# Kernel tuning notes

Hardware: AMD Instinct MI355X
Metric: run time of the kernel (lower is better)

## Reference

```python
import jax, jax.numpy as jnp
import numpy as np

N = 100000      # nodes
E = 1600000     # nnz of precomputed A^K (avg degree 16)
D = 64          # in_feats
C = 64          # n_classes
LN_EPS = 1e-5


def setup_inputs() -> dict:
    key = jax.random.key(0)
    ks = jax.random.split(key, 8)
    feat = jax.random.normal(ks[0], (N, D), dtype=jnp.float32)
    feat_ori = jax.random.normal(ks[1], (N, D), dtype=jnp.float32)
    row = jax.random.randint(ks[2], (E,), 0, N)
    col = jax.random.randint(ks[3], (E,), 0, N)
    adj_vals = jax.random.uniform(ks[4], (E,), dtype=jnp.float32)
    # Linear params (xavier_uniform weight, zero bias)
    limit = float(np.sqrt(6.0 / (D + C)))
    W = jax.random.uniform(ks[5], (C, D), dtype=jnp.float32, minval=-limit, maxval=limit)
    b = jnp.zeros((C,), dtype=jnp.float32)
    # LayerNorm params
    gamma = jnp.ones((C,), dtype=jnp.float32)
    beta = jnp.zeros((C,), dtype=jnp.float32)
    return {"feat": feat, "feat_ori": feat_ori, "row": row, "col": col,
            "adj_vals": adj_vals, "W": W, "b": b, "gamma": gamma, "beta": beta}


def reference(feat, feat_ori, row, col, adj_vals, W, b, gamma, beta):
    # NOTE: in the source, h = (1-alpha)*feat + alpha*feat_ori is dead code
    # (immediately overwritten by the SpMM of raw feat), so it is omitted.
    # SpMM: h[i] = sum_{e: row[e]=i} adj_vals[e] * feat[col[e]]   -> [N, D]
    msgs = adj_vals[:, None] * feat[col]            # [E, D] gather + scale
    h = jax.ops.segment_sum(msgs, row, num_segments=N)  # [N, D] scatter-add
    # Dense Linear: [N, D] @ [D, C] + [C]
    h = jnp.einsum('nd,cd->nc', h, W) + b
    # LayerNorm over last dim
    mu = jnp.mean(h, axis=-1, keepdims=True)
    var = jnp.mean(jnp.square(h - mu), axis=-1, keepdims=True)
    h = (h - mu) * jax.lax.rsqrt(var + LN_EPS) * gamma + beta
    return h
```

## Files before the change

### kernel.cpp

```cpp
#include <hip/hip_runtime.h>


typedef unsigned int u32;
typedef unsigned short u16;
typedef unsigned long long u64;
#define RFL(x) __builtin_amdgcn_readfirstlane(x)

#define NBLKC 64
#define MAXBK 2048
#define CAP 2048

__device__ __forceinline__ float bf2f(u16 v) {
    return __uint_as_float((u32)v << 16);
}
__device__ __forceinline__ u16 f2bf(float f) {
    u32 b = __float_as_uint(f);
    return (u16)((b + 0x7FFFu + ((b >> 16) & 1u)) >> 16);
}

__global__ __launch_bounds__(256) void k_bhist(const int* __restrict__ row,
                                               u32* __restrict__ hist2d,
                                               int E, int NBK, int CH) {
    __shared__ u32 cnt[MAXBK];
    int tid = threadIdx.x;
    for (int i = tid; i < NBK; i += 256) cnt[i] = 0;
    __syncthreads();
    int e0 = blockIdx.x * CH;
    int e1 = e0 + CH; if (e1 > E) e1 = E;
    int ev = e1 & ~3;
    for (int i = e0 + tid * 4; i < ev; i += 1024) {
        int4 r = *reinterpret_cast<const int4*>(&row[i]);
        atomicAdd(&cnt[(u32)r.x >> 6], 1u);
        atomicAdd(&cnt[(u32)r.y >> 6], 1u);
        atomicAdd(&cnt[(u32)r.z >> 6], 1u);
        atomicAdd(&cnt[(u32)r.w >> 6], 1u);
    }
    { int i = ev + tid; if (i < e1) atomicAdd(&cnt[(u32)row[i] >> 6], 1u); }
    __syncthreads();
    u32* dst = hist2d + (size_t)blockIdx.x * NBK;
    for (int i = tid; i < NBK; i += 256) dst[i] = cnt[i];
}

__device__ __forceinline__ u32 blk_scan256(u32 v, u32* wsum, u32& total) {
    int lane = threadIdx.x & 63, wid = threadIdx.x >> 6;
    u32 incl = v;
#pragma unroll
    for (int o = 1; o < 64; o <<= 1) {
        u32 u = __shfl_up(incl, o);
        if (lane >= o) incl += u;
    }
    if (lane == 63) wsum[wid] = incl;
    __syncthreads();
    u32 woff = 0;
    for (int w = 0; w < wid; ++w) woff += wsum[w];
    total = wsum[0] + wsum[1] + wsum[2] + wsum[3];
    __syncthreads();
    return woff + incl - v;
}

__global__ __launch_bounds__(256) void k_bscan(u32* __restrict__ hist2d,
                                               u32* __restrict__ btot,
                                               int NBLK, int NBK) {
    __shared__ u32 wsum[4];
    int bkt = blockIdx.x;
    u32 carry = 0;
    for (int r = 0; r < NBLK; r += 256) {
        int blk = r + threadIdx.x;
        u32 v = (blk < NBLK) ? hist2d[(size_t)blk * NBK + bkt] : 0;
        u32 tot;
        u32 ex = blk_scan256(v, wsum, tot);
        if (blk < NBLK) hist2d[(size_t)blk * NBK + bkt] = ex + carry;
        carry += tot;
    }
    if (threadIdx.x == 0) btot[bkt] = carry;
}

__global__ __launch_bounds__(256) void k_scanb2(const u32* __restrict__ btot,
                                                u32* __restrict__ bbase,
                                                int NBK, int E) {
    __shared__ u32 wsum[4];
    u32 carry = 0;
    for (int r = 0; r < NBK; r += 256) {
        int i = r + threadIdx.x;
        u32 v = (i < NBK) ? btot[i] : 0;
        u32 tot;
        u32 ex = blk_scan256(v, wsum, tot);
        if (i < NBK) bbase[i] = ex + carry;
        carry += tot;
    }
    if (threadIdx.x == 0) bbase[NBK] = (u32)E;
}

__global__ __launch_bounds__(512) void k_scatgemm(
    const int* __restrict__ row, const int* __restrict__ col,
    const float* __restrict__ vals, const u32* __restrict__ hist2d,
    const u32* __restrict__ bbase, u64* __restrict__ epair1,
    const float* __restrict__ feat, const float* __restrict__ W,
    u16* __restrict__ G, int E, int N, int NBK, int NBLK, int CH)
{
    __shared__ __align__(16) u32 smem[8192];
    int tid = threadIdx.x;
    if ((int)blockIdx.x < NBLK) {
        u32* lbase = smem;
        u32* lcnt  = smem + NBK;
        int blk = blockIdx.x;
        const u32* hrow = hist2d + (size_t)blk * NBK;
        for (int i = tid; i < NBK; i += 512) {
            lbase[i] = bbase[i] + hrow[i];
            lcnt[i] = 0;
        }
        __syncthreads();
        int e0 = blk * CH;
        int e1 = e0 + CH; if (e1 > E) e1 = E;
        int ev = e1 & ~3;
        for (int i = e0 + tid * 4; i < ev; i += 2048) {
            int4 r = *reinterpret_cast<const int4*>(&row[i]);
            int4 c = *reinterpret_cast<const int4*>(&col[i]);
            float4 v = *reinterpret_cast<const float4*>(&vals[i]);
            u32 k0 = (u32)r.x >> 6, k1 = (u32)r.y >> 6;
            u32 k2 = (u32)r.z >> 6, k3 = (u32)r.w >> 6;
            u32 q0 = atomicAdd(&lcnt[k0], 1u);
            u32 q1 = atomicAdd(&lcnt[k1], 1u);
            u32 q2 = atomicAdd(&lcnt[k2], 1u);
            u32 q3 = atomicAdd(&lcnt[k3], 1u);
            epair1[lbase[k0] + q0] = (u64)((u32)c.x | (((u32)r.x & 63u) << 26))
                                   | ((u64)__float_as_uint(v.x) << 32);
            epair1[lbase[k1] + q1] = (u64)((u32)c.y | (((u32)r.y & 63u) << 26))
                                   | ((u64)__float_as_uint(v.y) << 32);
            epair1[lbase[k2] + q2] = (u64)((u32)c.z | (((u32)r.z & 63u) << 26))
                                   | ((u64)__float_as_uint(v.z) << 32);
            epair1[lbase[k3] + q3] = (u64)((u32)c.w | (((u32)r.w & 63u) << 26))
                                   | ((u64)__float_as_uint(v.w) << 32);
        }
        {
            int i = ev + tid;
            if (i < e1) {
                u32 r = (u32)row[i];
                u32 k = r >> 6;
                u32 q = atomicAdd(&lcnt[k], 1u);
                epair1[lbase[k] + q] = (u64)((u32)col[i] | ((r & 63u) << 26))
                                     | ((u64)__float_as_uint(vals[i]) << 32);
            }
        }
    } else {
        float* fs = (float*)smem;
        int lane = tid & 63, wid = tid >> 6;
        int n0 = ((int)blockIdx.x - NBLK) * 128;
        int valid = N - n0; if (valid > 128) valid = 128;
        int elems = valid * 64;
        for (int idx = tid * 4; idx < elems; idx += 2048)
            *reinterpret_cast<float4*>(&fs[idx]) =
                *reinterpret_cast<const float4*>(&feat[(size_t)n0 * 64 + idx]);
        float wr[64];
#pragma unroll
        for (int d4 = 0; d4 < 16; ++d4) {
            float4 w4 = *reinterpret_cast<const float4*>(&W[lane * 64 + d4 * 4]);
            wr[d4 * 4 + 0] = w4.x; wr[d4 * 4 + 1] = w4.y;
            wr[d4 * 4 + 2] = w4.z; wr[d4 * 4 + 3] = w4.w;
        }
        __syncthreads();
        for (int j = 0; j < 16; ++j) {
            int r = wid * 16 + j;
            if (r >= valid) break;
            float oa[4] = {0.f, 0.f, 0.f, 0.f};
#pragma unroll
            for (int d4 = 0; d4 < 16; ++d4) {
                float4 h4 = *reinterpret_cast<const float4*>(&fs[r * 64 + d4 * 4]);
                oa[d4 & 3] = fmaf(h4.x, wr[d4 * 4 + 0],
                            fmaf(h4.y, wr[d4 * 4 + 1],
                            fmaf(h4.z, wr[d4 * 4 + 2],
                            fmaf(h4.w, wr[d4 * 4 + 3], oa[d4 & 3]))));
            }
            G[(size_t)(n0 + r) * 64 + lane] = f2bf((oa[0] + oa[1]) + (oa[2] + oa[3]));
        }
    }
}

__global__ __launch_bounds__(256) void k_node2(
    const u16* __restrict__ G, const u64* __restrict__ epair1,
    const u32* __restrict__ bbase, const float* __restrict__ bias,
    const float* __restrict__ gamma, const float* __restrict__ beta,
    float* __restrict__ out, int N)
{
    __shared__ u64 sp[CAP];
    __shared__ u32 cnt[64], base[64], cnt2[64];
    int tid = threadIdx.x, lane = tid & 63, wid = tid >> 6;
    int bkt = blockIdx.x;
    if (tid < 64) { cnt[tid] = 0; cnt2[tid] = 0; }
    __syncthreads();
    int s = RFL((int)bbase[bkt]);
    int t = RFL((int)bbase[bkt + 1]);
    int m = t - s;
    bool fits = (m <= CAP);

    const u32* meta1 = (const u32*)epair1;
    for (int i = s + tid; i < t; i += 256)
        atomicAdd(&cnt[meta1[2 * (size_t)i] >> 26], 1u);
    __syncthreads();
    if (tid < 64) {
        u32 v = cnt[tid];
        u32 incl = v;
#pragma unroll
        for (int o = 1; o < 64; o <<= 1) {
            u32 u = __shfl_up(incl, o);
            if (tid >= o) incl += u;
        }
        base[tid] = incl - v;
    }
    __syncthreads();
    if (fits) {
        for (int i = s + tid; i < t; i += 256) {
            u64 p = epair1[i];
            u32 mm = (u32)p;
            u32 r = mm >> 26;
            u32 rank = atomicAdd(&cnt2[r], 1u);
            sp[base[r] + rank] = (p & 0xFFFFFFFF00000000ull) | (u64)(mm & 0x03FFFFFFu);
        }
    }
    __syncthreads();

    int rbase = bkt << 6;
    for (int j = 0; j < 16; ++j) {
        int r = wid * 16 + j;
        int n = rbase + r;
        if (n >= N) break;
        float acc0 = 0.f, acc1 = 0.f;
        if (fits) {
            int e0 = base[r], e1 = base[r] + cnt[r];
            int i = e0;
            for (; i + 8 <= e1; i += 8) {
                u64 p0 = sp[i],     p1 = sp[i + 1];
                u64 p2 = sp[i + 2], p3 = sp[i + 3];
                u64 p4 = sp[i + 4], p5 = sp[i + 5];
                u64 p6 = sp[i + 6], p7 = sp[i + 7];
                u32 c0 = RFL((u32)p0), b0 = RFL((u32)(p0 >> 32));
                u32 c1 = RFL((u32)p1), b1 = RFL((u32)(p1 >> 32));
                u32 c2 = RFL((u32)p2), b2 = RFL((u32)(p2 >> 32));
                u32 c3 = RFL((u32)p3), b3 = RFL((u32)(p3 >> 32));
                u32 c4 = RFL((u32)p4), b4 = RFL((u32)(p4 >> 32));
                u32 c5 = RFL((u32)p5), b5 = RFL((u32)(p5 >> 32));
                u32 c6 = RFL((u32)p6), b6 = RFL((u32)(p6 >> 32));
                u32 c7 = RFL((u32)p7), b7 = RFL((u32)(p7 >> 32));
                float g0 = bf2f(G[((size_t)c0 << 6) | lane]);
                float g1 = bf2f(G[((size_t)c1 << 6) | lane]);
                float g2 = bf2f(G[((size_t)c2 << 6) | lane]);
                float g3 = bf2f(G[((size_t)c3 << 6) | lane]);
                float g4 = bf2f(G[((size_t)c4 << 6) | lane]);
                float g5 = bf2f(G[((size_t)c5 << 6) | lane]);
                float g6 = bf2f(G[((size_t)c6 << 6) | lane]);
                float g7 = bf2f(G[((size_t)c7 << 6) | lane]);
                acc0 = fmaf(__uint_as_float(b0), g0, acc0);
                acc1 = fmaf(__uint_as_float(b1), g1, acc1);
                acc0 = fmaf(__uint_as_float(b2), g2, acc0);
                acc1 = fmaf(__uint_as_float(b3), g3, acc1);
                acc0 = fmaf(__uint_as_float(b4), g4, acc0);
                acc1 = fmaf(__uint_as_float(b5), g5, acc1);
                acc0 = fmaf(__uint_as_float(b6), g6, acc0);
                acc1 = fmaf(__uint_as_float(b7), g7, acc1);
            }
            for (; i < e1; ++i) {
                u64 p = sp[i];
                u32 c = RFL((u32)p), b = RFL((u32)(p >> 32));
                acc0 = fmaf(__uint_as_float(b), bf2f(G[((size_t)c << 6) | lane]), acc0);
            }
        } else {
            for (int i = s; i < t; ++i) {
                u64 p = epair1[i];
                u32 mm = RFL((u32)p);
                if ((int)(mm >> 26) == r) {
                    u32 b = RFL((u32)(p >> 32));
                    acc0 = fmaf(__uint_as_float(b),
                                bf2f(G[((size_t)(mm & 0x03FFFFFFu) << 6) | lane]), acc0);
                }
            }
        }
        float o = acc0 + acc1 + bias[lane];

        float ssum = o;
#pragma unroll
        for (int off = 32; off; off >>= 1) ssum += __shfl_xor(ssum, off);
        float mu = ssum * 0.015625f;
        float dv = o - mu;
        float vs = dv * dv;
#pragma unroll
        for (int off = 32; off; off >>= 1) vs += __shfl_xor(vs, off);
        float inv = rsqrtf(vs * 0.015625f + 1e-5f);
        out[((size_t)n << 6) + lane] = dv * inv * gamma[lane] + beta[lane];
    }
}

extern "C" void kernel_launch(void* const* d_in, const int* in_sizes, int n_in,
                              void* d_out, int out_size, void* d_ws, size_t ws_size,
                              hipStream_t stream) {
    const float* feat  = (const float*)d_in[0];
    const int*   row   = (const int*)d_in[2];
    const int*   col   = (const int*)d_in[3];
    const float* vals  = (const float*)d_in[4];
    const float* W     = (const float*)d_in[5];
    const float* bias  = (const float*)d_in[6];
    const float* gamma = (const float*)d_in[7];
    const float* beta  = (const float*)d_in[8];
    float* out = (float*)d_out;

    const int D = 64;
    int N = in_sizes[0] / D;
    int E = in_sizes[2];

    int NBK  = (N + 63) / 64;
    int NBLK = NBLKC;
    int CH   = (((E + NBLK - 1) / NBLK) + 3) & ~3;
    int NG   = (N + 127) / 128;

    char* ws = (char*)d_ws;
    u16*   G      = (u16*)ws;
    size_t off1   = (((size_t)N * 128) + 255) & ~(size_t)255;
    u64*   epair1 = (u64*)(ws + off1);
    size_t off2   = off1 + (((size_t)E * 8 + 255) & ~(size_t)255);
    u32*   hist2d = (u32*)(ws + off2);
    size_t off3   = off2 + (((size_t)NBLK * NBK * 4 + 255) & ~(size_t)255);
    u32*   btot   = (u32*)(ws + off3);
    u32*   bbase  = btot + NBK;

    k_bhist   <<<NBLK, 256, 0, stream>>>(row, hist2d, E, NBK, CH);
    k_bscan   <<<NBK, 256, 0, stream>>>(hist2d, btot, NBLK, NBK);
    k_scanb2  <<<1, 256, 0, stream>>>(btot, bbase, NBK, E);
    k_scatgemm<<<NBLK + NG, 512, 0, stream>>>(row, col, vals, hist2d, bbase,
                                              epair1, feat, W, G,
                                              E, N, NBK, NBLK, CH);
    k_node2   <<<NBK, 256, 0, stream>>>(G, epair1, bbase, bias, gamma, beta,
                                        out, N);
}
```

Measured before the change: 136.3 us.

## Locally counting-sort edge chunks in LDS before coalesced bucket scatter

Each scatter block now builds a local histogram of its edge chunk, scans it, and counting-sorts edge indices into shared memory. It then writes edges to global buckets in sorted order, so neighbouring threads write neighbouring addresses instead of random 8-byte stores. The block count goes from a fixed 64 to about E/12500 (128 for this size), so each chunk fits in the u16 LDS index buffer. The cost is re-reading row/col/vals several times, extra LDS passes and more barriers, and hist2d sizing now depends on the larger block count.

```diff
diff --git a/kernel.cpp b/kernel.cpp
--- a/kernel.cpp
+++ b/kernel.cpp
@@ -6,7 +6,8 @@
 typedef unsigned long long u64;
 #define RFL(x) __builtin_amdgcn_readfirstlane(x)
 
-#define NBLKC 64
+#define CHMAX 12500
+#define SCAP 14336
 #define MAXBK 2048
 #define CAP 2048
 
@@ -91,6 +92,25 @@
     if (threadIdx.x == 0) bbase[NBK] = (u32)E;
 }
 
+__device__ __forceinline__ u32 blk_scan512(u32 v, u32* wsum, u32& total) {
+    int lane = threadIdx.x & 63, wid = threadIdx.x >> 6;
+    u32 incl = v;
+#pragma unroll
+    for (int o = 1; o < 64; o <<= 1) {
+        u32 u = __shfl_up(incl, o);
+        if (lane >= o) incl += u;
+    }
+    if (lane == 63) wsum[wid] = incl;
+    __syncthreads();
+    u32 woff = 0;
+    for (int w = 0; w < wid; ++w) woff += wsum[w];
+    total = 0;
+#pragma unroll
+    for (int w = 0; w < 8; ++w) total += wsum[w];
+    __syncthreads();
+    return woff + incl - v;
+}
+
 __global__ __launch_bounds__(512) void k_scatgemm(
     const int* __restrict__ row, const int* __restrict__ col,
     const float* __restrict__ vals, const u32* __restrict__ hist2d,
@@ -98,11 +118,14 @@
     const float* __restrict__ feat, const float* __restrict__ W,
     u16* __restrict__ G, int E, int N, int NBK, int NBLK, int CH)
 {
-    __shared__ __align__(16) u32 smem[8192];
+    __shared__ __align__(16) u32 smem[SCAP / 2 + 3 * MAXBK + 8];
     int tid = threadIdx.x;
     if ((int)blockIdx.x < NBLK) {
-        u32* lbase = smem;
-        u32* lcnt  = smem + NBK;
+        u16* sidx  = (u16*)smem;
+        u32* lbase = smem + SCAP / 2;
+        u32* locb  = lbase + MAXBK;
+        u32* lcnt  = locb + MAXBK;
+        u32* wsum  = lcnt + MAXBK;
         int blk = blockIdx.x;
         const u32* hrow = hist2d + (size_t)blk * NBK;
         for (int i = tid; i < NBK; i += 512) {
@@ -112,35 +135,37 @@
         __syncthreads();
         int e0 = blk * CH;
         int e1 = e0 + CH; if (e1 > E) e1 = E;
-        int ev = e1 & ~3;
-        for (int i = e0 + tid * 4; i < ev; i += 2048) {
-            int4 r = *reinterpret_cast<const int4*>(&row[i]);
-            int4 c = *reinterpret_cast<const int4*>(&col[i]);
-            float4 v = *reinterpret_cast<const float4*>(&vals[i]);
-            u32 k0 = (u32)r.x >> 6, k1 = (u32)r.y >> 6;
-            u32 k2 = (u32)r.z >> 6, k3 = (u32)r.w >> 6;
-            u32 q0 = atomicAdd(&lcnt[k0], 1u);
-            u32 q1 = atomicAdd(&lcnt[k1], 1u);
-            u32 q2 = atomicAdd(&lcnt[k2], 1u);
-            u32 q3 = atomicAdd(&lcnt[k3], 1u);
-            epair1[lbase[k0] + q0] = (u64)((u32)c.x | (((u32)r.x & 63u) << 26))
-                                   | ((u64)__float_as_uint(v.x) << 32);
-            epair1[lbase[k1] + q1] = (u64)((u32)c.y | (((u32)r.y & 63u) << 26))
-                                   | ((u64)__float_as_uint(v.y) << 32);
-            epair1[lbase[k2] + q2] = (u64)((u32)c.z | (((u32)r.z & 63u) << 26))
-                                   | ((u64)__float_as_uint(v.z) << 32);
-            epair1[lbase[k3] + q3] = (u64)((u32)c.w | (((u32)r.w & 63u) << 26))
-                                   | ((u64)__float_as_uint(v.w) << 32);
-        }
+        int m = e1 - e0;
+        for (int e = e0 + tid; e < e1; e += 512)
+            atomicAdd(&lcnt[(u32)row[e] >> 6], 1u);
+        __syncthreads();
         {
-            int i = ev + tid;
-            if (i < e1) {
-                u32 r = (u32)row[i];
-                u32 k = r >> 6;
-                u32 q = atomicAdd(&lcnt[k], 1u);
-                epair1[lbase[k] + q] = (u64)((u32)col[i] | ((r & 63u) << 26))
-                                     | ((u64)__float_as_uint(vals[i]) << 32);
-            }
+            u32 carry = 0;
+            for (int r = 0; r < NBK; r += 512) {
+                int i = r + tid;
+                u32 v = (i < NBK) ? lcnt[i] : 0;
+                u32 tot;
+                u32 ex = blk_scan512(v, wsum, tot);
+                if (i < NBK) locb[i] = ex + carry;
+                carry += tot;
+            }
+        }
+        __syncthreads();
+        for (int i = tid; i < NBK; i += 512) lcnt[i] = 0;
+        __syncthreads();
+        for (int e = e0 + tid; e < e1; e += 512) {
+            u32 b = (u32)row[e] >> 6;
+            u32 rank = atomicAdd(&lcnt[b], 1u);
+            sidx[locb[b] + rank] = (u16)(e - e0);
+        }
+        __syncthreads();
+        for (int i = tid; i < m; i += 512) {
+            int e = e0 + (int)sidx[i];
+            u32 r = (u32)row[e];
+            u32 b = r >> 6;
+            u32 dst = lbase[b] + ((u32)i - locb[b]);
+            epair1[dst] = (u64)((u32)col[e] | ((r & 63u) << 26))
+                        | ((u64)__float_as_uint(vals[e]) << 32);
         }
     } else {
         float* fs = (float*)smem;
@@ -307,7 +332,8 @@
     int E = in_sizes[2];
 
     int NBK  = (N + 63) / 64;
-    int NBLK = NBLKC;
+    int NBLK = (E + CHMAX - 1) / CHMAX;
+    if (NBLK < 1) NBLK = 1;
     int CH   = (((E + NBLK - 1) / NBLK) + 3) & ~3;
     int NG   = (N + 127) / 128;
 
```

Result: slower. 150.7 us (+10.6%).
